# Performance work log

Measured on AMD Instinct MI355X. Metric: run time of the kernel, lower is better.

Reference implementation:

```python
import jax, jax.numpy as jnp
import numpy as np

E = 1024; H = 16; D = E // H; MAX_LEN = 512; B = 4; N = 1024
EPS = 1e-5
NEG_INF = float('-inf')


def layernorm(x, g, b):
    mu = jnp.mean(x, axis=-1, keepdims=True)
    var = jnp.mean((x - mu) ** 2, axis=-1, keepdims=True)
    return (x - mu) * jax.lax.rsqrt(var + EPS) * g + b


def rel_bias(seq_len, rel_pos):
    # rel_pos: (H, MAX_LEN). bias[h,i,j] = rel_pos[h, i-j] if 0<=i-j<MAX_LEN else -inf
    pos = jnp.arange(seq_len)
    rel = pos[:, None] - pos[None, :]                     # (N, N)
    valid = (rel >= 0) & (rel < rel_pos.shape[-1])
    idx = jnp.clip(rel, 0, rel_pos.shape[-1] - 1)
    gathered = rel_pos[:, idx]                            # (H, N, N)
    return jnp.where(valid[None], gathered, NEG_INF)


def setup_inputs() -> dict:
    key = jax.random.key(0)
    ks = jax.random.split(key, 12)
    s = 0.02
    return {
        'x': jax.random.normal(ks[0], (B, N, E), jnp.float32),
        'rel_pos': jax.random.normal(ks[1], (H, MAX_LEN), jnp.float32),
        'in_proj_w': jax.random.normal(ks[2], (3 * E, E), jnp.float32) * s,
        'in_proj_b': jnp.zeros((3 * E,), jnp.float32),
        'out_w': jax.random.normal(ks[3], (E, E), jnp.float32) * s,
        'out_b': jnp.zeros((E,), jnp.float32),
        'w1': jax.random.normal(ks[4], (4 * E, E), jnp.float32) * s,
        'b1': jnp.zeros((4 * E,), jnp.float32),
        'w2': jax.random.normal(ks[5], (E, 4 * E), jnp.float32) * s,
        'b2': jnp.zeros((E,), jnp.float32),
        'ln1_g': jnp.ones((E,), jnp.float32),
        'ln1_b': jnp.zeros((E,), jnp.float32),
        'ln2_g': jnp.ones((E,), jnp.float32),
        'ln2_b': jnp.zeros((E,), jnp.float32),
    }


def reference(x, rel_pos, in_proj_w, in_proj_b, out_w, out_b,
              w1, b1, w2, b2, ln1_g, ln1_b, ln2_g, ln2_b):
    b, n, e = x.shape
    xn = layernorm(x, ln1_g, ln1_b)
    qkv = xn @ in_proj_w.T + in_proj_b                    # (B, N, 3E)
    q, k, v = jnp.split(qkv, 3, axis=-1)
    # (B, N, E) -> (B, H, N, D)
    def heads(t):
        return t.reshape(b, n, H, D).transpose(0, 2, 1, 3)
    q, k, v = heads(q), heads(k), heads(v)
    bias = rel_bias(n, rel_pos)                           # (H, N, N)
    scores = jnp.einsum('bhnd,bhmd->bhnm', q, k) / np.sqrt(D) + bias[None]
    attn = jax.nn.softmax(scores, axis=-1)
    o = jnp.einsum('bhnm,bhmd->bhnd', attn, v)            # (B, H, N, D)
    o = o.transpose(0, 2, 1, 3).reshape(b, n, e)
    x = x + o @ out_w.T + out_b
    xm = layernorm(x, ln2_g, ln2_b)
    h = jax.nn.relu(xm @ w1.T + b1)
    return x + h @ w2.T + b2
```

## Files before the change

kernel.cpp:

```cpp
#include <hip/hip_runtime.h>
#include <math.h>

#define BB 4
#define NN 1024
#define EE 1024
#define HH 16
#define DD 64
#define MAXLEN 512
#define EPS 1e-5f

typedef __attribute__((ext_vector_type(8))) __bf16 bf16x8;
typedef __attribute__((ext_vector_type(4))) float floatx4;
typedef __attribute__((ext_vector_type(8))) unsigned short ushort8;

#define SWAIT(s) asm volatile("s_waitcnt " s ::: "memory")
#define SCHEDBAR() __builtin_amdgcn_sched_barrier(0)

__device__ __forceinline__ unsigned short f2bf(float f) {
    unsigned u = __float_as_uint(f);
    u += 0x7fffu + ((u >> 16) & 1u);
    return (unsigned short)(u >> 16);
}

template <int MAXR>
__device__ __forceinline__ void vm_wait_rt(int rem) {
    if (rem >= MAXR) {
        if constexpr (MAXR <= 0)      SWAIT("vmcnt(0)");
        else if constexpr (MAXR == 1) SWAIT("vmcnt(4)");
        else if constexpr (MAXR == 2) SWAIT("vmcnt(8)");
        else if constexpr (MAXR == 3) SWAIT("vmcnt(12)");
        else if constexpr (MAXR == 4) SWAIT("vmcnt(16)");
        else if constexpr (MAXR == 5) SWAIT("vmcnt(20)");
        else                          SWAIT("vmcnt(24)");
        return;
    }
    if (rem <= 0) { SWAIT("vmcnt(0)"); return; }
    if (rem == 1) { SWAIT("vmcnt(4)"); return; }
    if constexpr (MAXR >= 3) { if (rem == 2) { SWAIT("vmcnt(8)");  return; } }
    if constexpr (MAXR >= 4) { if (rem == 3) { SWAIT("vmcnt(12)"); return; } }
    if constexpr (MAXR >= 5) { if (rem == 4) { SWAIT("vmcnt(16)"); return; } }
    if constexpr (MAXR >= 6) { if (rem == 5) { SWAIT("vmcnt(20)"); return; } }
}

__global__ __launch_bounds__(256) void f2bf_kernel(const float* __restrict__ in,
                                                   unsigned short* __restrict__ out,
                                                   int n4) {
    int i = blockIdx.x * 256 + threadIdx.x;
    if (i < n4) {
        float4 v = ((const float4*)in)[i];
        ushort4 o;
        o.x = f2bf(v.x); o.y = f2bf(v.y); o.z = f2bf(v.z); o.w = f2bf(v.w);
        ((ushort4*)out)[i] = o;
    }
}

__global__ __launch_bounds__(256) void ln_kernel(const float* __restrict__ x,
                                                 const float* __restrict__ g,
                                                 const float* __restrict__ b,
                                                 unsigned short* __restrict__ out) {
    const int row = blockIdx.x;
    const float* xr = x + (size_t)row * EE;
    float s = 0.f, s2 = 0.f;
    for (int j = threadIdx.x; j < EE; j += 256) {
        float v = xr[j];
        s += v; s2 += v * v;
    }
    for (int off = 32; off > 0; off >>= 1) {
        s  += __shfl_xor(s, off);
        s2 += __shfl_xor(s2, off);
    }
    __shared__ float red[8];
    const int wave = threadIdx.x >> 6, lane = threadIdx.x & 63;
    if (lane == 0) { red[wave] = s; red[4 + wave] = s2; }
    __syncthreads();
    s  = red[0] + red[1] + red[2] + red[3];
    s2 = red[4] + red[5] + red[6] + red[7];
    const float mu  = s * (1.0f / EE);
    const float var = s2 * (1.0f / EE) - mu * mu;
    const float inv = rsqrtf(var + EPS);
    unsigned short* orow = out + (size_t)row * EE;
    for (int j = threadIdx.x; j < EE; j += 256) {
        orow[j] = f2bf((xr[j] - mu) * inv * g[j] + b[j]);
    }
}

template <int BM, int BN, int WMG, int WNG, int DEPTH, int VARIANT, bool XSWZ>
__global__ __launch_bounds__(WMG * WNG * 64, (WMG * WNG == 8) ? 2 : 1)
void gemm_pl_kernel(
    const unsigned short* __restrict__ A,
    const unsigned short* __restrict__ W,
    const float* __restrict__ bias,
    const float* res, void* Cout, int Nc, int K) {
    constexpr int NW  = WMG * WNG;
    constexpr int WTM = BM / WMG;
    constexpr int WTN = BN / WNG;
    constexpr int MR  = WTM / 16;
    constexpr int NR  = WTN / 16;
    static_assert(NR == 4, "NR must be 4");
    constexpr int SA = BM / (16 * NW);
    constexpr int SB = BN / (16 * NW);
    static_assert(SA == 2 && SB == 2, "stage count must be 2+2");
    static_assert((DEPTH & (DEPTH - 1)) == 0, "DEPTH must be pow2");
    constexpr int DMASK = DEPTH - 1;

    __shared__ unsigned short smem[DEPTH][(BM + BN) * 32];

    const int tid  = threadIdx.x;
    const int lane = tid & 63;
    const int wv   = tid >> 6;
    const int wm   = wv / WNG;
    const int wn   = wv % WNG;

    int bx = blockIdx.x, by = blockIdx.y;
    if (XSWZ) {
        const int gx  = gridDim.x;
        const int nwg = gx * gridDim.y;
        const int lin = by * gx + bx;
        const int sl  = (lin & 7) * (nwg >> 3) + (lin >> 3);
        bx = sl % gx; by = sl / gx;
    }
    const int row0 = by * BM;
    const int col0 = bx * BN;
    const int NT   = K >> 5;

    const int srow = lane >> 2;
    const int sq   = ((lane & 3) ^ ((lane >> 3) & 3)) * 8;
    const unsigned short* Ag = A + (size_t)(row0 + srow) * K + sq;
    const unsigned short* Wg = W + (size_t)(col0 + srow) * K + sq;

    auto stage = [&](int t) {
        unsigned short* dst = &smem[t & DMASK][0];
#pragma unroll
        for (int s = 0; s < SA; ++s) {
            const int r = (wv + s * NW) * 16;
            __builtin_amdgcn_global_load_lds(
                (const __attribute__((address_space(1))) unsigned int*)(Ag + (size_t)r * K + t * 32),
                (__attribute__((address_space(3))) unsigned int*)(dst + r * 32), 16, 0, 0);
        }
#pragma unroll
        for (int s = 0; s < SB; ++s) {
            const int r = (wv + s * NW) * 16;
            __builtin_amdgcn_global_load_lds(
                (const __attribute__((address_space(1))) unsigned int*)(Wg + (size_t)r * K + t * 32),
                (__attribute__((address_space(3))) unsigned int*)(dst + (BM + r) * 32), 16, 0, 0);
        }
    };

    const int frow = lane & 15;
    const int quad = lane >> 4;
    const int rq   = (quad ^ ((frow >> 1) & 3)) * 8;
    const int abase = (wm * WTM + frow) * 32 + rq;
    const int bbase = (BM + wn * WTN + frow) * 32 + rq;

    floatx4 acc[MR][4];
#pragma unroll
    for (int m = 0; m < MR; ++m)
#pragma unroll
        for (int n = 0; n < 4; ++n) acc[m][n] = (floatx4){0.f, 0.f, 0.f, 0.f};

    bf16x8 afA[MR], afB[MR];

#pragma unroll
    for (int pt = 0; pt < DEPTH - 1; ++pt) stage(pt);
    vm_wait_rt<DEPTH - 2>(DEPTH - 2);
    __builtin_amdgcn_s_barrier();
    SCHEDBAR();
#pragma unroll
    for (int m = 0; m < MR; ++m)
        afA[m] = *(const bf16x8*)(&smem[0][0] + abase + m * (16 * 32));

#define GEMM_BODY(T, AFC, AFN, TAIL)                                           \
    {                                                                          \
        const int t_ = (T);                                                    \
        if (!(TAIL)) vm_wait_rt<DEPTH - 2>(NT - 2 - t_);                       \
        __builtin_amdgcn_s_barrier();                                          \
        SCHEDBAR();                                                            \
        if (t_ + DEPTH - 1 < NT) stage(t_ + DEPTH - 1);                        \
        const unsigned short* buf_ = &smem[t_ & DMASK][0];                     \
        bf16x8 bfr0 = *(const bf16x8*)(buf_ + bbase);                          \
        bf16x8 bfr1 = *(const bf16x8*)(buf_ + bbase + 16 * 32);                \
        SCHEDBAR();                                                            \
        bf16x8 bfr2 = *(const bf16x8*)(buf_ + bbase + 32 * 32);                \
        bf16x8 bfr3 = *(const bf16x8*)(buf_ + bbase + 48 * 32);                \
        if (!(TAIL)) {                                                         \
            const unsigned short* nbuf_ = &smem[(t_ + 1) & DMASK][0];          \
            _Pragma("unroll")                                                  \
            for (int m = 0; m < MR; ++m)                                       \
                AFN[m] = *(const bf16x8*)(nbuf_ + abase + m * (16 * 32));      \
        }                                                                      \
        SCHEDBAR();                                                            \
        if (TAIL) { SWAIT("lgkmcnt(2)"); }                                     \
        else { if constexpr (MR == 8) SWAIT("lgkmcnt(10)");                    \
               else SWAIT("lgkmcnt(6)"); }                                     \
        SCHEDBAR();                                                            \
        __builtin_amdgcn_s_setprio(1);                                         \
        _Pragma("unroll")                                                      \
        for (int m = 0; m < MR; ++m) {                                         \
            acc[m][0] = __builtin_amdgcn_mfma_f32_16x16x32_bf16(               \
                AFC[m], bfr0, acc[m][0], 0, 0, 0);                             \
            acc[m][1] = __builtin_amdgcn_mfma_f32_16x16x32_bf16(               \
                AFC[m], bfr1, acc[m][1], 0, 0, 0);                             \
        }                                                                      \
        SCHEDBAR();                                                            \
        if (TAIL) { SWAIT("lgkmcnt(0)"); }                                     \
        else { if constexpr (MR == 8) SWAIT("lgkmcnt(8)");                     \
               else SWAIT("lgkmcnt(4)"); }                                     \
        SCHEDBAR();                                                            \
        _Pragma("unroll")                                                      \
        for (int m = 0; m < MR; ++m) {                                         \
            acc[m][2] = __builtin_amdgcn_mfma_f32_16x16x32_bf16(               \
                AFC[m], bfr2, acc[m][2], 0, 0, 0);                             \
            acc[m][3] = __builtin_amdgcn_mfma_f32_16x16x32_bf16(               \
                AFC[m], bfr3, acc[m][3], 0, 0, 0);                             \
        }                                                                      \
        __builtin_amdgcn_s_setprio(0);                                         \
        SCHEDBAR();                                                            \
    }

    int t = 0;
    for (; t < NT - 2; t += 2) {
        GEMM_BODY(t,     afA, afB, false);
        GEMM_BODY(t + 1, afB, afA, false);
    }
    GEMM_BODY(NT - 2, afA, afB, false);
    GEMM_BODY(NT - 1, afB, afA, true);
#undef GEMM_BODY

    const int crow = (lane >> 4) * 4;
    const int ccol = lane & 15;
#pragma unroll
    for (int n = 0; n < 4; ++n) {
        const int nn = col0 + wn * WTN + n * 16 + ccol;
        const float bv = bias[nn];
#pragma unroll
        for (int m = 0; m < MR; ++m) {
#pragma unroll
            for (int r = 0; r < 4; ++r) {
                const int mm = row0 + wm * WTM + m * 16 + crow + r;
                float v = acc[m][n][r] + bv;
                if (VARIANT == 1) v = fmaxf(v, 0.f);
                if (VARIANT == 2) {
                    ((float*)Cout)[(size_t)mm * Nc + nn] = v + res[(size_t)mm * Nc + nn];
                } else {
                    ((unsigned short*)Cout)[(size_t)mm * Nc + nn] = f2bf(v);
                }
            }
        }
    }
}

__global__ __launch_bounds__(256) void attn_mfma_kernel(
    const unsigned short* __restrict__ qkv,
    const float* __restrict__ rel_pos,
    unsigned short* __restrict__ o) {
    __shared__ unsigned short K_s[2][64][32];
    __shared__ unsigned short V_s[64][72];
    __shared__ unsigned short P_s[4][2][16][32];
    __shared__ float rel_s[MAXLEN];

    const int qt = blockIdx.x, h = blockIdx.y, b = blockIdx.z;
    const int q0 = qt * 64;
    const int tid  = threadIdx.x;
    const int lane = tid & 63;
    const int w    = tid >> 6;
    const int quad = lane >> 4;
    const int c15  = lane & 15;

    rel_s[tid]       = rel_pos[h * MAXLEN + tid];
    rel_s[tid + 256] = rel_pos[h * MAXLEN + tid + 256];

    const size_t rowstride = 3 * EE;
    const size_t base_q = (size_t)(b * NN) * rowstride + h * DD;
    const size_t base_k = base_q + EE;
    const size_t base_v = base_q + 2 * EE;

    bf16x8 aq[2];
    {
        const unsigned short* qrow =
            qkv + base_q + (size_t)(q0 + w * 16 + c15) * rowstride + quad * 8;
        aq[0] = *(const bf16x8*)(qrow);
        aq[1] = *(const bf16x8*)(qrow + 32);
    }

    floatx4 Oacc[4];
#pragma unroll
    for (int j = 0; j < 4; ++j) Oacc[j] = (floatx4){0.f, 0.f, 0.f, 0.f};
    float m_r[4], l_r[4];
#pragma unroll
    for (int r = 0; r < 4; ++r) { m_r[r] = -1e30f; l_r[r] = 0.f; }

    const int jlo = max(0, q0 - (MAXLEN - 1));
    const int c0 = jlo >> 6;
    const int c1 = (q0 + 63) >> 6;

    for (int cc = c0; cc <= c1; ++cc) {
        const int jb0 = cc << 6;
        __syncthreads();

        {
            const int krow = w * 16 + (lane >> 2);
            const int dofs = (lane & 3) * 8;
            const unsigned short* gk =
                qkv + base_k + (size_t)(jb0 + krow) * rowstride + dofs;
            __builtin_amdgcn_global_load_lds(
                (const __attribute__((address_space(1))) unsigned int*)gk,
                (__attribute__((address_space(3))) unsigned int*)&K_s[0][w * 16][0],
                16, 0, 0);
            __builtin_amdgcn_global_load_lds(
                (const __attribute__((address_space(1))) unsigned int*)(gk + 32),
                (__attribute__((address_space(3))) unsigned int*)&K_s[1][w * 16][0],
                16, 0, 0);
        }
        {
            const int key = lane;
            const int d0  = w * 16;
            const unsigned short* gv =
                qkv + base_v + (size_t)(jb0 + key) * rowstride + d0;
            ushort8 va = *(const ushort8*)(gv);
            ushort8 vb = *(const ushort8*)(gv + 8);
#pragma unroll
            for (int ii = 0; ii < 8; ++ii) V_s[d0 + ii][key] = va[ii];
#pragma unroll
            for (int ii = 0; ii < 8; ++ii) V_s[d0 + 8 + ii][key] = vb[ii];
        }
        __syncthreads();

        floatx4 S[4];
#pragma unroll
        for (int jb = 0; jb < 4; ++jb) {
            S[jb] = (floatx4){0.f, 0.f, 0.f, 0.f};
            bf16x8 bk0 = *(const bf16x8*)&K_s[0][jb * 16 + c15][quad * 8];
            bf16x8 bk1 = *(const bf16x8*)&K_s[1][jb * 16 + c15][quad * 8];
            S[jb] = __builtin_amdgcn_mfma_f32_16x16x32_bf16(aq[0], bk0, S[jb], 0, 0, 0);
            S[jb] = __builtin_amdgcn_mfma_f32_16x16x32_bf16(aq[1], bk1, S[jb], 0, 0, 0);
        }

        const int i_base = q0 + w * 16 + quad * 4;
        float sv[4][4];
        float mc[4] = {-1e30f, -1e30f, -1e30f, -1e30f};
#pragma unroll
        for (int jb = 0; jb < 4; ++jb) {
            const int jg = jb0 + jb * 16 + c15;
#pragma unroll
            for (int r = 0; r < 4; ++r) {
                const int rel = (i_base + r) - jg;
                float s;
                if (rel >= 0 && rel < MAXLEN) s = S[jb][r] * 0.125f + rel_s[rel];
                else                          s = -1e30f;
                sv[jb][r] = s;
                mc[r] = fmaxf(mc[r], s);
            }
        }
#pragma unroll
        for (int off = 1; off < 16; off <<= 1)
#pragma unroll
            for (int r = 0; r < 4; ++r) mc[r] = fmaxf(mc[r], __shfl_xor(mc[r], off));

        float alpha[4], psum[4];
#pragma unroll
        for (int r = 0; r < 4; ++r) {
            const float mn = fmaxf(m_r[r], mc[r]);
            alpha[r] = __expf(m_r[r] - mn);
            m_r[r] = mn;
            psum[r] = 0.f;
        }
#pragma unroll
        for (int jb = 0; jb < 4; ++jb)
#pragma unroll
            for (int r = 0; r < 4; ++r) {
                const float p = __expf(sv[jb][r] - m_r[r]);
                sv[jb][r] = p;
                psum[r] += p;
            }
#pragma unroll
        for (int off = 1; off < 16; off <<= 1)
#pragma unroll
            for (int r = 0; r < 4; ++r) psum[r] += __shfl_xor(psum[r], off);
#pragma unroll
        for (int r = 0; r < 4; ++r) l_r[r] = l_r[r] * alpha[r] + psum[r];
#pragma unroll
        for (int jb = 0; jb < 4; ++jb)
#pragma unroll
            for (int r = 0; r < 4; ++r) Oacc[jb][r] *= alpha[r];

#pragma unroll
        for (int jb = 0; jb < 4; ++jb)
#pragma unroll
            for (int r = 0; r < 4; ++r)
                P_s[w][jb >> 1][quad * 4 + r][(jb & 1) * 16 + c15] = f2bf(sv[jb][r]);

        bf16x8 ap0 = *(const bf16x8*)&P_s[w][0][c15][quad * 8];
        bf16x8 ap1 = *(const bf16x8*)&P_s[w][1][c15][quad * 8];

#pragma unroll
        for (int jd = 0; jd < 4; ++jd) {
            bf16x8 bv0 = *(const bf16x8*)&V_s[jd * 16 + c15][quad * 8];
            bf16x8 bv1 = *(const bf16x8*)&V_s[jd * 16 + c15][32 + quad * 8];
            Oacc[jd] = __builtin_amdgcn_mfma_f32_16x16x32_bf16(ap0, bv0, Oacc[jd], 0, 0, 0);
            Oacc[jd] = __builtin_amdgcn_mfma_f32_16x16x32_bf16(ap1, bv1, Oacc[jd], 0, 0, 0);
        }
    }

    float inv[4];
#pragma unroll
    for (int r = 0; r < 4; ++r) inv[r] = 1.0f / l_r[r];
#pragma unroll
    for (int jd = 0; jd < 4; ++jd) {
#pragma unroll
        for (int r = 0; r < 4; ++r) {
            const int row = q0 + w * 16 + quad * 4 + r;
            const int col = h * DD + jd * 16 + c15;
            o[(size_t)(b * NN + row) * EE + col] = f2bf(Oacc[jd][r] * inv[r]);
        }
    }
}

extern "C" void kernel_launch(void* const* d_in, const int* in_sizes, int n_in,
                              void* d_out, int out_size, void* d_ws, size_t ws_size,
                              hipStream_t stream) {
    const float* x         = (const float*)d_in[0];
    const float* rel_pos   = (const float*)d_in[1];
    const float* in_proj_w = (const float*)d_in[2];
    const float* in_proj_b = (const float*)d_in[3];
    const float* out_w     = (const float*)d_in[4];
    const float* out_b     = (const float*)d_in[5];
    const float* w1        = (const float*)d_in[6];
    const float* b1        = (const float*)d_in[7];
    const float* w2        = (const float*)d_in[8];
    const float* b2        = (const float*)d_in[9];
    const float* ln1_g     = (const float*)d_in[10];
    const float* ln1_b     = (const float*)d_in[11];
    const float* ln2_g     = (const float*)d_in[12];
    const float* ln2_b     = (const float*)d_in[13];
    float* out = (float*)d_out;

    char* wsb = (char*)d_ws;
    const size_t MB = 1024 * 1024;
    unsigned short* wqkv_b = (unsigned short*)(wsb + 0);
    unsigned short* wout_b = (unsigned short*)(wsb + 6 * MB);
    unsigned short* w1_b   = (unsigned short*)(wsb + 8 * MB);
    unsigned short* w2_b   = (unsigned short*)(wsb + 16 * MB);
    unsigned short* xn_b   = (unsigned short*)(wsb + 24 * MB);
    unsigned short* qkv_b  = (unsigned short*)(wsb + 32 * MB);
    unsigned short* h_b    = (unsigned short*)(wsb + 32 * MB);
    unsigned short* o_b    = (unsigned short*)(wsb + 56 * MB);

    const int Mrows = BB * NN;

    f2bf_kernel<<<(3 * EE * EE / 4 + 255) / 256, 256, 0, stream>>>(in_proj_w, wqkv_b, 3 * EE * EE / 4);
    f2bf_kernel<<<(EE * EE / 4 + 255) / 256, 256, 0, stream>>>(out_w, wout_b, EE * EE / 4);
    f2bf_kernel<<<(4 * EE * EE / 4 + 255) / 256, 256, 0, stream>>>(w1, w1_b, 4 * EE * EE / 4);
    f2bf_kernel<<<(4 * EE * EE / 4 + 255) / 256, 256, 0, stream>>>(w2, w2_b, 4 * EE * EE / 4);

    ln_kernel<<<Mrows, 256, 0, stream>>>(x, ln1_g, ln1_b, xn_b);
    gemm_pl_kernel<256, 256, 2, 4, 4, 0, true><<<dim3(3 * EE / 256, Mrows / 256), 512, 0, stream>>>(
        xn_b, wqkv_b, in_proj_b, nullptr, qkv_b, 3 * EE, EE);
    attn_mfma_kernel<<<dim3(NN / 64, HH, BB), 256, 0, stream>>>(qkv_b, rel_pos, o_b);
    gemm_pl_kernel<128, 128, 2, 2, 8, 2, true><<<dim3(EE / 128, Mrows / 128), 256, 0, stream>>>(
        o_b, wout_b, out_b, x, out, EE, EE);
    ln_kernel<<<Mrows, 256, 0, stream>>>(out, ln2_g, ln2_b, xn_b);
    gemm_pl_kernel<256, 256, 2, 4, 4, 1, true><<<dim3(4 * EE / 256, Mrows / 256), 512, 0, stream>>>(
        xn_b, w1_b, b1, nullptr, h_b, 4 * EE, EE);
    gemm_pl_kernel<128, 128, 2, 2, 8, 2, true><<<dim3(EE / 128, Mrows / 128), 256, 0, stream>>>(
        h_b, w2_b, b2, out, out, EE, 4 * EE);
}
```

Measured before the change: 351.6 us.

## Add intra-block split-K GEMM for out-proj and FFN2 with LDS reduction

```diff
diff --git a/kernel.cpp b/kernel.cpp
--- a/kernel.cpp
+++ b/kernel.cpp
@@ -249,6 +249,162 @@
     }
 }
 
+__global__ __launch_bounds__(512, 2) void gemm_kh_kernel(
+    const unsigned short* __restrict__ A,
+    const unsigned short* __restrict__ W,
+    const float* __restrict__ bias,
+    const float* res, float* Cout, int Nc, int K) {
+    __shared__ unsigned short smem[4][16384];
+
+    const int tid  = threadIdx.x;
+    const int lane = tid & 63;
+    const int wv   = tid >> 6;
+    const int wk   = wv >> 2;
+    const int wm   = (wv >> 1) & 1;
+    const int wn   = wv & 1;
+
+    int bx = blockIdx.x, by = blockIdx.y;
+    {
+        const int gx  = gridDim.x;
+        const int nwg = gx * gridDim.y;
+        const int lin = by * gx + bx;
+        const int sl  = (lin & 7) * (nwg >> 3) + (lin >> 3);
+        bx = sl % gx; by = sl / gx;
+    }
+    const int row0 = by * 128;
+    const int col0 = bx * 128;
+    const int NT   = K >> 6;
+
+    const int srow = lane >> 3;
+    const int sq   = ((lane & 7) ^ ((lane >> 3) & 7)) * 8;
+    const unsigned short* Ag = A + (size_t)(row0 + srow) * K + sq;
+    const unsigned short* Wg = W + (size_t)(col0 + srow) * K + sq;
+
+    auto stage = [&](int t) {
+        unsigned short* dst = &smem[t & 3][0];
+#pragma unroll
+        for (int s = 0; s < 2; ++s) {
+            const int r = (wv + s * 8) * 8;
+            __builtin_amdgcn_global_load_lds(
+                (const __attribute__((address_space(1))) unsigned int*)(Ag + (size_t)r * K + t * 64),
+                (__attribute__((address_space(3))) unsigned int*)(dst + r * 64), 16, 0, 0);
+        }
+#pragma unroll
+        for (int s = 0; s < 2; ++s) {
+            const int r = (wv + s * 8) * 8;
+            __builtin_amdgcn_global_load_lds(
+                (const __attribute__((address_space(1))) unsigned int*)(Wg + (size_t)r * K + t * 64),
+                (__attribute__((address_space(3))) unsigned int*)(dst + 8192 + r * 64), 16, 0, 0);
+        }
+    };
+
+    const int frow = lane & 15;
+    const int quad = lane >> 4;
+    const int phys = ((wk * 4 + quad) ^ (frow & 7)) * 8;
+    const int abase = (wm * 64 + frow) * 64 + phys;
+    const int bbase = 8192 + (wn * 64 + frow) * 64 + phys;
+
+    floatx4 acc[4][4];
+#pragma unroll
+    for (int m = 0; m < 4; ++m)
+#pragma unroll
+        for (int n = 0; n < 4; ++n) acc[m][n] = (floatx4){0.f, 0.f, 0.f, 0.f};
+
+    bf16x8 afA[4], afB[4];
+
+    stage(0); stage(1); stage(2);
+    SWAIT("vmcnt(8)");
+    __builtin_amdgcn_s_barrier();
+    SCHEDBAR();
+#pragma unroll
+    for (int m = 0; m < 4; ++m)
+        afA[m] = *(const bf16x8*)(&smem[0][0] + abase + m * 1024);
+
+#define KH_BODY(T, AFC, AFN, TAIL)                                             \
+    {                                                                          \
+        const int t_ = (T);                                                    \
+        if (!(TAIL)) vm_wait_rt<2>(NT - 2 - t_);                               \
+        __builtin_amdgcn_s_barrier();                                          \
+        SCHEDBAR();                                                            \
+        if (t_ + 3 < NT) stage(t_ + 3);                                        \
+        const unsigned short* buf_ = &smem[t_ & 3][0];                         \
+        bf16x8 bfr0 = *(const bf16x8*)(buf_ + bbase);                          \
+        bf16x8 bfr1 = *(const bf16x8*)(buf_ + bbase + 1024);                   \
+        SCHEDBAR();                                                            \
+        bf16x8 bfr2 = *(const bf16x8*)(buf_ + bbase + 2048);                   \
+        bf16x8 bfr3 = *(const bf16x8*)(buf_ + bbase + 3072);                   \
+        if (!(TAIL)) {                                                         \
+            const unsigned short* nbuf_ = &smem[(t_ + 1) & 3][0];              \
+            _Pragma("unroll")                                                  \
+            for (int m = 0; m < 4; ++m)                                        \
+                AFN[m] = *(const bf16x8*)(nbuf_ + abase + m * 1024);           \
+        }                                                                      \
+        SCHEDBAR();                                                            \
+        if (TAIL) { SWAIT("lgkmcnt(2)"); } else { SWAIT("lgkmcnt(6)"); }       \
+        SCHEDBAR();                                                            \
+        __builtin_amdgcn_s_setprio(1);                                         \
+        _Pragma("unroll")                                                      \
+        for (int m = 0; m < 4; ++m) {                                          \
+            acc[m][0] = __builtin_amdgcn_mfma_f32_16x16x32_bf16(               \
+                AFC[m], bfr0, acc[m][0], 0, 0, 0);                             \
+            acc[m][1] = __builtin_amdgcn_mfma_f32_16x16x32_bf16(               \
+                AFC[m], bfr1, acc[m][1], 0, 0, 0);                             \
+        }                                                                      \
+        SCHEDBAR();                                                            \
+        if (TAIL) { SWAIT("lgkmcnt(0)"); } else { SWAIT("lgkmcnt(4)"); }       \
+        SCHEDBAR();                                                            \
+        _Pragma("unroll")                                                      \
+        for (int m = 0; m < 4; ++m) {                                          \
+            acc[m][2] = __builtin_amdgcn_mfma_f32_16x16x32_bf16(               \
+                AFC[m], bfr2, acc[m][2], 0, 0, 0);                             \
+            acc[m][3] = __builtin_amdgcn_mfma_f32_16x16x32_bf16(               \
+                AFC[m], bfr3, acc[m][3], 0, 0, 0);                             \
+        }                                                                      \
+        __builtin_amdgcn_s_setprio(0);                                         \
+        SCHEDBAR();                                                            \
+    }
+
+    int t = 0;
+    for (; t < NT - 2; t += 2) {
+        KH_BODY(t,     afA, afB, false);
+        KH_BODY(t + 1, afB, afA, false);
+    }
+    KH_BODY(NT - 2, afA, afB, false);
+    KH_BODY(NT - 1, afB, afA, true);
+#undef KH_BODY
+
+    __syncthreads();
+    float* pbuf = (float*)&smem[0][0];
+    const int pair = wm * 2 + wn;
+    if (wk == 1) {
+#pragma unroll
+        for (int m = 0; m < 4; ++m)
+#pragma unroll
+            for (int n = 0; n < 4; ++n)
+                *(floatx4*)&pbuf[pair * 4096 + (m * 4 + n) * 256 + lane * 4] = acc[m][n];
+    }
+    __syncthreads();
+    if (wk == 0) {
+        const int crow = (lane >> 4) * 4;
+        const int ccol = lane & 15;
+#pragma unroll
+        for (int n = 0; n < 4; ++n) {
+            const int nn = col0 + wn * 64 + n * 16 + ccol;
+            const float bv = bias[nn];
+#pragma unroll
+            for (int m = 0; m < 4; ++m) {
+                floatx4 p = *(const floatx4*)&pbuf[pair * 4096 + (m * 4 + n) * 256 + lane * 4];
+#pragma unroll
+                for (int r = 0; r < 4; ++r) {
+                    const int mm = row0 + wm * 64 + m * 16 + crow + r;
+                    Cout[(size_t)mm * Nc + nn] =
+                        acc[m][n][r] + p[r] + bv + res[(size_t)mm * Nc + nn];
+                }
+            }
+        }
+    }
+}
+
 __global__ __launch_bounds__(256) void attn_mfma_kernel(
     const unsigned short* __restrict__ qkv,
     const float* __restrict__ rel_pos,
@@ -456,11 +612,11 @@
     gemm_pl_kernel<256, 256, 2, 4, 4, 0, true><<<dim3(3 * EE / 256, Mrows / 256), 512, 0, stream>>>(
         xn_b, wqkv_b, in_proj_b, nullptr, qkv_b, 3 * EE, EE);
     attn_mfma_kernel<<<dim3(NN / 64, HH, BB), 256, 0, stream>>>(qkv_b, rel_pos, o_b);
-    gemm_pl_kernel<128, 128, 2, 2, 8, 2, true><<<dim3(EE / 128, Mrows / 128), 256, 0, stream>>>(
+    gemm_kh_kernel<<<dim3(EE / 128, Mrows / 128), 512, 0, stream>>>(
         o_b, wout_b, out_b, x, out, EE, EE);
     ln_kernel<<<Mrows, 256, 0, stream>>>(out, ln2_g, ln2_b, xn_b);
     gemm_pl_kernel<256, 256, 2, 4, 4, 1, true><<<dim3(4 * EE / 256, Mrows / 256), 512, 0, stream>>>(
         xn_b, w1_b, b1, nullptr, h_b, 4 * EE, EE);
-    gemm_pl_kernel<128, 128, 2, 2, 8, 2, true><<<dim3(EE / 128, Mrows / 128), 256, 0, stream>>>(
+    gemm_kh_kernel<<<dim3(EE / 128, Mrows / 128), 512, 0, stream>>>(
         h_b, w2_b, b2, out, out, EE, 4 * EE);
 }
```

Measured after the change: 340.0 us. 1.03x faster.
